# Kernel optimization log

Hardware: AMD Instinct MI355X
Metric: run time of the kernel (lower is better)

The kernel has to match this reference:

```python
import jax, jax.numpy as jnp
import numpy as np

N_NODES = 256
BATCH = 8
N_IN = 64
N_HID = 128
N_OUT = 64


def _incidence():
    # fully connected graph without self-loops (standard NRI setup)
    off_diag = np.ones((N_NODES, N_NODES)) - np.eye(N_NODES)
    recv_idx, send_idx = np.where(off_diag)  # each [E], E = N*(N-1)
    eye = np.eye(N_NODES, dtype=np.float32)
    rel_rec = eye[recv_idx]   # [E, N] one-hot
    rel_send = eye[send_idx]  # [E, N] one-hot
    return jnp.asarray(rel_rec), jnp.asarray(rel_send)


def setup_inputs() -> dict:
    key = jax.random.key(0)
    k_x, k_w1, k_w2 = jax.random.split(key, 3)
    rel_rec, rel_send = _incidence()
    x = jax.random.normal(k_x, (BATCH, N_NODES, N_IN), dtype=jnp.float32)
    # torch.nn.Linear weights: [out_features, in_features]
    W1 = jax.random.normal(k_w1, (N_HID, 2 * N_IN), dtype=jnp.float32) / np.sqrt(2 * N_IN)
    b1 = jnp.zeros((N_HID,), dtype=jnp.float32)
    W2 = jax.random.normal(k_w2, (N_OUT, N_HID), dtype=jnp.float32) / np.sqrt(N_HID)
    b2 = jnp.zeros((N_OUT,), dtype=jnp.float32)
    return {"x": x, "rel_rec": rel_rec, "rel_send": rel_send,
            "W1": W1, "b1": b1, "W2": W2, "b2": b2}


def reference(x, rel_rec, rel_send, W1, b1, W2, b2):
    # node2edge: dense one-hot matmuls (gather of node features per edge)
    receivers = jnp.einsum('en,bnf->bef', rel_rec, x)   # [B, E, n_in]
    senders = jnp.einsum('en,bnf->bef', rel_send, x)    # [B, E, n_in]
    edges = jnp.concatenate([senders, receivers], axis=-1)  # [B, E, 2*n_in]
    # 2-layer MLP: Linear -> ReLU -> Linear (torch Linear: y = x @ W.T + b)
    h = jax.nn.relu(jnp.einsum('bef,hf->beh', edges, W1) + b1)
    out = jnp.einsum('beh,oh->beo', h, W2) + b2          # [B, E, n_out]
    return out
```

## Files before the change

### kernel.cpp

```cpp
#include <hip/hip_runtime.h>


using frag_t  = __attribute__((ext_vector_type(8))) short;
using f32x4   = __attribute__((ext_vector_type(4))) float;
using ushort8 = __attribute__((ext_vector_type(8))) unsigned short;

__device__ inline unsigned short f2bf(float f) {
    union { float f; unsigned u; } v; v.f = f;
    unsigned r = v.u + 0x7fffu + ((v.u >> 16) & 1u);
    return (unsigned short)(r >> 16);
}

__device__ inline ushort8 pack8(f32x4 a, f32x4 b) {
    ushort8 o;
    o[0] = f2bf(a[0]); o[1] = f2bf(a[1]); o[2] = f2bf(a[2]); o[3] = f2bf(a[3]);
    o[4] = f2bf(b[0]); o[5] = f2bf(b[1]); o[6] = f2bf(b[2]); o[7] = f2bf(b[3]);
    return o;
}

__device__ inline frag_t packfrag(f32x4 a, f32x4 b) {
    union { ushort8 u; frag_t f; } v; v.u = pack8(a, b); return v.f;
}

__global__ __launch_bounds__(256)
void nri_mlp_fused(const float* __restrict__ x,
                   const float* __restrict__ W1,
                   const float* __restrict__ b1,
                   const float* __restrict__ W2,
                   const float* __restrict__ b2,
                   float* __restrict__ out) {
    __shared__ unsigned short W1s[128 * 128];
    __shared__ unsigned short W2s[64 * 128];

    const int tid  = threadIdx.x;
    const int wave = tid >> 6;
    const int lane = tid & 63;
    const int quad = lane >> 4;
    const int n16  = lane & 15;

    const int bx = blockIdx.x;
    const int b  = bx / 255;
    const int eb = (bx - b * 255) * 256;
    const int e0 = eb + wave * 64;

    const float* xb = x + b * (256 * 64);

    #pragma unroll
    for (int i = 0; i < 8; ++i) {
        int cid  = tid + i * 256;
        int row  = cid >> 4;
        int c    = cid & 15;
        int slot = c ^ (row & 7);
        const float* s = W1 + row * 128 + c * 8;
        *(ushort8*)&W1s[row * 128 + slot * 8] =
            pack8(*(const f32x4*)s, *(const f32x4*)(s + 4));
    }
    #pragma unroll
    for (int i = 0; i < 4; ++i) {
        int cid  = tid + i * 256;
        int row  = cid >> 4;
        int c    = cid & 15;
        int slot = c ^ (row & 7);
        int base = 32 * (c >> 2) + 4 * (c & 3);
        const float* s = W2 + row * 128 + base;
        *(ushort8*)&W2s[row * 128 + slot * 8] =
            pack8(*(const f32x4*)s, *(const f32x4*)(s + 16));
    }
    __syncthreads();

    f32x4 b1v4[8];
    #pragma unroll
    for (int c = 0; c < 8; ++c) b1v4[c] = *(const f32x4*)(b1 + c * 16 + quad * 4);
    f32x4 b2v4[4];
    #pragma unroll
    for (int c2 = 0; c2 < 4; ++c2) b2v4[c2] = *(const f32x4*)(b2 + c2 * 16 + quad * 4);

    #pragma unroll 1
    for (int t = 0; t < 4; ++t) {
        int e    = e0 + t * 16 + n16;
        int recv = e / 255;
        int kk   = e - recv * 255;
        int send = kk + (kk >= recv ? 1 : 0);

        frag_t af[4];
        #pragma unroll
        for (int ks = 0; ks < 4; ++ks) {
            int node = (ks < 2) ? send : recv;
            const float* s = xb + node * 64 + ((ks & 1) * 4 + quad) * 8;
            af[ks] = packfrag(*(const f32x4*)s, *(const f32x4*)(s + 4));
        }

        f32x4 acc[8];
        #pragma unroll
        for (int c = 0; c < 8; ++c) acc[c] = b1v4[c];
        #pragma unroll
        for (int ks = 0; ks < 4; ++ks) {
            #pragma unroll
            for (int c = 0; c < 8; ++c) {
                int row  = c * 16 + n16;
                int slot = (ks * 4 + quad) ^ (row & 7);
                frag_t w1 = *(const frag_t*)&W1s[row * 128 + slot * 8];
                acc[c] = __builtin_amdgcn_mfma_f32_16x16x32_bf16(w1, af[ks], acc[c], 0, 0, 0);
            }
        }

        frag_t hf[4];
        #pragma unroll
        for (int ks = 0; ks < 4; ++ks) {
            f32x4 lo = acc[2 * ks], hi = acc[2 * ks + 1];
            #pragma unroll
            for (int ri = 0; ri < 4; ++ri) {
                lo[ri] = lo[ri] > 0.f ? lo[ri] : 0.f;
                hi[ri] = hi[ri] > 0.f ? hi[ri] : 0.f;
            }
            hf[ks] = packfrag(lo, hi);
        }

        f32x4 acc2[4];
        #pragma unroll
        for (int c2 = 0; c2 < 4; ++c2) acc2[c2] = b2v4[c2];
        #pragma unroll
        for (int ks = 0; ks < 4; ++ks) {
            #pragma unroll
            for (int c2 = 0; c2 < 4; ++c2) {
                int row  = c2 * 16 + n16;
                int slot = (ks * 4 + quad) ^ (row & 7);
                frag_t w2 = *(const frag_t*)&W2s[row * 128 + slot * 8];
                acc2[c2] = __builtin_amdgcn_mfma_f32_16x16x32_bf16(w2, hf[ks], acc2[c2], 0, 0, 0);
            }
        }

        float* ob = out + ((long)b * 65280 + e) * 64;
        #pragma unroll
        for (int c2 = 0; c2 < 4; ++c2)
            *(f32x4*)&ob[c2 * 16 + quad * 4] = acc2[c2];
    }
}

extern "C" void kernel_launch(void* const* d_in, const int* in_sizes, int n_in,
                              void* d_out, int out_size, void* d_ws, size_t ws_size,
                              hipStream_t stream) {
    const float* x  = (const float*)d_in[0];
    const float* W1 = (const float*)d_in[3];
    const float* b1 = (const float*)d_in[4];
    const float* W2 = (const float*)d_in[5];
    const float* b2 = (const float*)d_in[6];
    (void)d_ws; (void)ws_size; (void)in_sizes; (void)n_in; (void)out_size;
    float* out = (float*)d_out;

    nri_mlp_fused<<<2040, 256, 0, stream>>>(x, W1, b1, W2, b2, out);
}
```

Before: 258.2 us.

## Switch MLP to 32x32x16 bf16 MFMA with per-group bias loads

Replaces the 16x16x32 MFMA tiling with 32x32x16 tiles, so each wave handles 32 edges per iteration over two iterations instead of 16 edges over four. The LDS weight layout and the W2 packing are reordered to match the new fragment layout. Biases are no longer kept in registers; they are added after accumulation by loading them from global memory, which lowers register pressure. The bf16 conversion now uses the HIP intrinsic. The larger MFMA shape should cut instruction count and LDS reads per FLOP, at the cost of a changed output store pattern and extra bias loads.

```diff
diff --git a/kernel.cpp b/kernel.cpp
--- a/kernel.cpp
+++ b/kernel.cpp
@@ -1,14 +1,16 @@
 #include <hip/hip_runtime.h>
+#include <hip/hip_bf16.h>
 
 
 using frag_t  = __attribute__((ext_vector_type(8))) short;
 using f32x4   = __attribute__((ext_vector_type(4))) float;
+using f32x16  = __attribute__((ext_vector_type(16))) float;
 using ushort8 = __attribute__((ext_vector_type(8))) unsigned short;
 
 __device__ inline unsigned short f2bf(float f) {
-    union { float f; unsigned u; } v; v.f = f;
-    unsigned r = v.u + 0x7fffu + ((v.u >> 16) & 1u);
-    return (unsigned short)(r >> 16);
+    union { __hip_bfloat16 h; unsigned short u; } v;
+    v.h = __float2bfloat16(f);
+    return v.u;
 }
 
 __device__ inline ushort8 pack8(f32x4 a, f32x4 b) {
@@ -21,6 +23,8 @@
 __device__ inline frag_t packfrag(f32x4 a, f32x4 b) {
     union { ushort8 u; frag_t f; } v; v.u = pack8(a, b); return v.f;
 }
+
+__device__ inline int swz(int row, int c) { return c ^ (row & 7); }
 
 __global__ __launch_bounds__(256)
 void nri_mlp_fused(const float* __restrict__ x,
@@ -35,8 +39,8 @@
     const int tid  = threadIdx.x;
     const int wave = tid >> 6;
     const int lane = tid & 63;
-    const int quad = lane >> 4;
-    const int n16  = lane & 15;
+    const int hi   = lane >> 5;
+    const int l5   = lane & 31;
 
     const int bx = blockIdx.x;
     const int b  = bx / 255;
@@ -50,9 +54,8 @@
         int cid  = tid + i * 256;
         int row  = cid >> 4;
         int c    = cid & 15;
-        int slot = c ^ (row & 7);
         const float* s = W1 + row * 128 + c * 8;
-        *(ushort8*)&W1s[row * 128 + slot * 8] =
+        *(ushort8*)&W1s[row * 128 + swz(row, c) * 8] =
             pack8(*(const f32x4*)s, *(const f32x4*)(s + 4));
     }
     #pragma unroll
@@ -60,80 +63,93 @@
         int cid  = tid + i * 256;
         int row  = cid >> 4;
         int c    = cid & 15;
-        int slot = c ^ (row & 7);
-        int base = 32 * (c >> 2) + 4 * (c & 3);
+        int base = 32 * (c >> 2) + 16 * ((c >> 1) & 1) + 4 * (c & 1);
         const float* s = W2 + row * 128 + base;
-        *(ushort8*)&W2s[row * 128 + slot * 8] =
-            pack8(*(const f32x4*)s, *(const f32x4*)(s + 16));
+        *(ushort8*)&W2s[row * 128 + swz(row, c) * 8] =
+            pack8(*(const f32x4*)s, *(const f32x4*)(s + 8));
     }
     __syncthreads();
 
-    f32x4 b1v4[8];
-    #pragma unroll
-    for (int c = 0; c < 8; ++c) b1v4[c] = *(const f32x4*)(b1 + c * 16 + quad * 4);
-    f32x4 b2v4[4];
-    #pragma unroll
-    for (int c2 = 0; c2 < 4; ++c2) b2v4[c2] = *(const f32x4*)(b2 + c2 * 16 + quad * 4);
-
     #pragma unroll 1
-    for (int t = 0; t < 4; ++t) {
-        int e    = e0 + t * 16 + n16;
+    for (int g = 0; g < 2; ++g) {
+        int e    = e0 + g * 32 + l5;
         int recv = e / 255;
         int kk   = e - recv * 255;
         int send = kk + (kk >= recv ? 1 : 0);
 
-        frag_t af[4];
+        frag_t af[8];
         #pragma unroll
-        for (int ks = 0; ks < 4; ++ks) {
-            int node = (ks < 2) ? send : recv;
-            const float* s = xb + node * 64 + ((ks & 1) * 4 + quad) * 8;
+        for (int ks = 0; ks < 8; ++ks) {
+            int node = (ks < 4) ? send : recv;
+            const float* s = xb + node * 64 + (ks & 3) * 16 + hi * 8;
             af[ks] = packfrag(*(const f32x4*)s, *(const f32x4*)(s + 4));
         }
 
-        f32x4 acc[8];
+        f32x16 acc[4];
         #pragma unroll
-        for (int c = 0; c < 8; ++c) acc[c] = b1v4[c];
+        for (int cb = 0; cb < 4; ++cb)
+            #pragma unroll
+            for (int r = 0; r < 16; ++r) acc[cb][r] = 0.f;
         #pragma unroll
-        for (int ks = 0; ks < 4; ++ks) {
+        for (int ks = 0; ks < 8; ++ks) {
+            int chunk = 2 * ks + hi;
             #pragma unroll
-            for (int c = 0; c < 8; ++c) {
-                int row  = c * 16 + n16;
-                int slot = (ks * 4 + quad) ^ (row & 7);
-                frag_t w1 = *(const frag_t*)&W1s[row * 128 + slot * 8];
-                acc[c] = __builtin_amdgcn_mfma_f32_16x16x32_bf16(w1, af[ks], acc[c], 0, 0, 0);
+            for (int cb = 0; cb < 4; ++cb) {
+                int row = 32 * cb + l5;
+                frag_t w1 = *(const frag_t*)&W1s[row * 128 + swz(row, chunk) * 8];
+                acc[cb] = __builtin_amdgcn_mfma_f32_32x32x16_bf16(w1, af[ks], acc[cb], 0, 0, 0);
             }
         }
 
-        frag_t hf[4];
+        const float* b1p = b1;
+        asm volatile("" : "+s"(b1p));
+        frag_t hf[8];
         #pragma unroll
-        for (int ks = 0; ks < 4; ++ks) {
-            f32x4 lo = acc[2 * ks], hi = acc[2 * ks + 1];
+        for (int cb = 0; cb < 4; ++cb) {
+            f32x4 t[4];
             #pragma unroll
-            for (int ri = 0; ri < 4; ++ri) {
-                lo[ri] = lo[ri] > 0.f ? lo[ri] : 0.f;
-                hi[ri] = hi[ri] > 0.f ? hi[ri] : 0.f;
+            for (int m = 0; m < 4; ++m) {
+                f32x4 bv = *(const f32x4*)(b1p + 32 * cb + 8 * m + 4 * hi);
+                #pragma unroll
+                for (int q = 0; q < 4; ++q) {
+                    float v = acc[cb][4 * m + q] + bv[q];
+                    t[m][q] = v > 0.f ? v : 0.f;
+                }
             }
-            hf[ks] = packfrag(lo, hi);
+            hf[2 * cb]     = packfrag(t[0], t[1]);
+            hf[2 * cb + 1] = packfrag(t[2], t[3]);
         }
 
-        f32x4 acc2[4];
+        f32x16 acc2[2];
         #pragma unroll
-        for (int c2 = 0; c2 < 4; ++c2) acc2[c2] = b2v4[c2];
+        for (int c2 = 0; c2 < 2; ++c2)
+            #pragma unroll
+            for (int r = 0; r < 16; ++r) acc2[c2][r] = 0.f;
         #pragma unroll
-        for (int ks = 0; ks < 4; ++ks) {
+        for (int ks = 0; ks < 8; ++ks) {
+            int chunk = 2 * ks + hi;
             #pragma unroll
-            for (int c2 = 0; c2 < 4; ++c2) {
-                int row  = c2 * 16 + n16;
-                int slot = (ks * 4 + quad) ^ (row & 7);
-                frag_t w2 = *(const frag_t*)&W2s[row * 128 + slot * 8];
-                acc2[c2] = __builtin_amdgcn_mfma_f32_16x16x32_bf16(w2, hf[ks], acc2[c2], 0, 0, 0);
+            for (int c2 = 0; c2 < 2; ++c2) {
+                int row = 32 * c2 + l5;
+                frag_t w2 = *(const frag_t*)&W2s[row * 128 + swz(row, chunk) * 8];
+                acc2[c2] = __builtin_amdgcn_mfma_f32_32x32x16_bf16(w2, hf[ks], acc2[c2], 0, 0, 0);
             }
         }
 
+        const float* b2p = b2;
+        asm volatile("" : "+s"(b2p));
         float* ob = out + ((long)b * 65280 + e) * 64;
         #pragma unroll
-        for (int c2 = 0; c2 < 4; ++c2)
-            *(f32x4*)&ob[c2 * 16 + quad * 4] = acc2[c2];
+        for (int c2 = 0; c2 < 2; ++c2) {
+            #pragma unroll
+            for (int m = 0; m < 4; ++m) {
+                f32x4 bv = *(const f32x4*)(b2p + 32 * c2 + 8 * m + 4 * hi);
+                f32x4 v;
+                #pragma unroll
+                for (int q = 0; q < 4; ++q) v[q] = acc2[c2][4 * m + q] + bv[q];
+                *(f32x4*)&ob[32 * c2 + 8 * m + 4 * hi] = v;
+            }
+        }
     }
 }
 
```

After: 259.7 us. Within noise of the previous version (+0.6%).
